# Kernel tuning notes

Measured on AMD Instinct MI355X. Metric: run time of the kernel, lower is better.

The kernel has to match this reference:

```python
import jax, jax.numpy as jnp
import numpy as np

ALPHA = 0.05


def setup_inputs() -> dict:
    key = jax.random.key(0)
    k1, k2, k3, k4 = jax.random.split(key, 4)
    B, C, D = 16384, 4096, 768
    logits = jax.random.normal(k1, (B, C), dtype=jnp.float32)
    targets = jax.random.randint(k2, (B,), 0, C, dtype=jnp.int64)
    prototypes = jax.random.normal(k3, (C, D), dtype=jnp.float32)
    boundaries = jax.random.uniform(k4, (C,), dtype=jnp.float32)
    return {"logits": logits, "targets": targets,
            "prototypes": prototypes, "boundaries": boundaries}


def _cross_entropy(logits, targets):
    # mean over batch of -log_softmax(logits)[target]
    logp = jax.nn.log_softmax(logits, axis=-1)
    nll = -jnp.take_along_axis(logp, targets[:, None], axis=-1)[:, 0]
    return jnp.mean(nll)


def _inter_class_constraint(prototypes, boundaries):
    C = prototypes.shape[0]
    # Gram matrix G[i, j] = p_i . p_j  replaces the O(C^2) python loop
    gram = prototypes @ prototypes.T                      # [C, C]
    diag = jnp.diagonal(gram)                             # p_i . p_i, [C]
    term1 = (1.0 - boundaries) * diag                     # [C], depends on i only
    term2 = (boundaries[None, :] - 1.0) * gram            # [C, C], b_j and G[i,j]
    constraint = term1[:, None] + term2                   # [C, C]
    off_diag = 1.0 - jnp.eye(C, dtype=constraint.dtype)
    ic_sum = jnp.sum(jax.nn.relu(constraint) * off_diag)
    count = C * (C - 1)
    return ic_sum / max(count, 1)


def reference(logits, targets, prototypes, boundaries):
    cls_loss = _cross_entropy(logits, targets)
    ic_loss = _inter_class_constraint(prototypes, boundaries)
    total_loss = cls_loss + ALPHA * ic_loss
    return (total_loss, cls_loss, ic_loss)
```

## Files before the change

kernel.cpp:

```cpp
#include <hip/hip_runtime.h>
#include <hip/hip_bf16.h>

#define NB 16384
#define NC 4096
#define ND 768
#define NT 32
#define NIC 528
#define CE_BLOCKS 2048

#define WS_NLLP 0
#define WS_ICP  16384
#define WS_T1   20480
#define WS_P16  36864


typedef __bf16 bf16x8 __attribute__((ext_vector_type(8)));
typedef float  f32x4  __attribute__((ext_vector_type(4)));

__device__ __forceinline__ unsigned short f2bf(float f) {
    return __builtin_bit_cast(unsigned short, __float2bfloat16(f));
}

template<bool PRECONV>
__global__ __launch_bounds__(256) void prep_kernel(const float* __restrict__ prot,
                                                   const float* __restrict__ bnd,
                                                   float* __restrict__ t1,
                                                   unsigned short* __restrict__ P16) {
    int w = threadIdx.x >> 6;
    int lane = threadIdx.x & 63;
    int row = blockIdx.x * 4 + w;
    const float4* rp = reinterpret_cast<const float4*>(prot + (size_t)row * ND);
    float ss = 0.f;
#pragma unroll
    for (int it = 0; it < 3; ++it) {
        int idx = it * 64 + lane;
        float4 v = rp[idx];
        ss += v.x * v.x + v.y * v.y + v.z * v.z + v.w * v.w;
        if (PRECONV) {
            ushort4 h;
            h.x = f2bf(v.x); h.y = f2bf(v.y); h.z = f2bf(v.z); h.w = f2bf(v.w);
            *reinterpret_cast<ushort4*>(P16 + (size_t)row * ND + idx * 4) = h;
        }
    }
#pragma unroll
    for (int off = 32; off; off >>= 1) ss += __shfl_xor(ss, off);
    if (lane == 0) t1[row] = (1.f - bnd[row]) * ss;
}

__global__ __launch_bounds__(256) void ce_kernel(const float* __restrict__ logits,
                                                 const int* __restrict__ targets,
                                                 double* __restrict__ nllp) {
    const int tid = threadIdx.x;
    const int w = tid >> 6, lane = tid & 63;
    const int b = blockIdx.x;
    float wave_nll = 0.f;
#pragma unroll
    for (int r = 0; r < 2; ++r) {
        const int row = b * 8 + w * 2 + r;
        const int t = targets[row];
        const float4* rp = reinterpret_cast<const float4*>(logits + (size_t)row * NC);
        const float xt = logits[(size_t)row * NC + t];
        float4 v[16];
#pragma unroll
        for (int k = 0; k < 16; ++k) v[k] = rp[lane + 64 * k];
        float m = -3.4e38f;
#pragma unroll
        for (int k = 0; k < 16; ++k)
            m = fmaxf(m, fmaxf(fmaxf(v[k].x, v[k].y), fmaxf(v[k].z, v[k].w)));
#pragma unroll
        for (int off = 32; off; off >>= 1) m = fmaxf(m, __shfl_xor(m, off));
        float s = 0.f;
#pragma unroll
        for (int k = 0; k < 16; ++k)
            s += __expf(v[k].x - m) + __expf(v[k].y - m) + __expf(v[k].z - m) + __expf(v[k].w - m);
#pragma unroll
        for (int off = 32; off; off >>= 1) s += __shfl_xor(s, off);
        wave_nll += m + __logf(s) - xt;
    }
    __shared__ float wp[4];
    if (lane == 0) wp[w] = wave_nll;
    __syncthreads();
    if (tid == 0) nllp[b] = (double)((wp[0] + wp[1]) + (wp[2] + wp[3]));
}

template<bool PRECONV>
__global__ __launch_bounds__(256) void ic_kernel(const unsigned short* __restrict__ P16,
                                                 const float* __restrict__ prot,
                                                 const float* __restrict__ bnd,
                                                 const float* __restrict__ t1,
                                                 float* __restrict__ icp) {
    __shared__ __bf16 As[128][72];
    __shared__ __bf16 Bs[128][72];
    const int tid = threadIdx.x;

    const int icid = blockIdx.x;
    int u = icid, bi = 0;
    while (u >= NT - bi) { u -= NT - bi; ++bi; }
    const int bj = bi + u;
    const bool diag = (bi == bj);
    const int row0 = bi * 128, col0 = bj * 128;

    const int lane = tid & 63, w = tid >> 6;
    const int fr = lane & 15, fq = lane >> 4;
    const int wrow = (w >> 1) * 64, wcol = (w & 1) * 64;

    f32x4 acc[4][4];
#pragma unroll
    for (int mi = 0; mi < 4; ++mi)
#pragma unroll
        for (int nj = 0; nj < 4; ++nj) acc[mi][nj] = (f32x4){0.f, 0.f, 0.f, 0.f};

    for (int kt = 0; kt < ND / 64; ++kt) {
        if (PRECONV) {
#pragma unroll
            for (int s2 = 0; s2 < 4; ++s2) {
                int c = tid + 256 * s2;
                int r = c >> 3, k8 = c & 7;
                uint4 va = *reinterpret_cast<const uint4*>(P16 + (size_t)(row0 + r) * ND + kt * 64 + k8 * 8);
                *reinterpret_cast<uint4*>(&As[r][k8 * 8]) = va;
                uint4 vb = *reinterpret_cast<const uint4*>(P16 + (size_t)(col0 + r) * ND + kt * 64 + k8 * 8);
                *reinterpret_cast<uint4*>(&Bs[r][k8 * 8]) = vb;
            }
        } else {
#pragma unroll
            for (int s2 = 0; s2 < 8; ++s2) {
                int c = tid + 256 * s2;
                int r = c >> 4, k4 = c & 15;
                float4 va = *reinterpret_cast<const float4*>(prot + (size_t)(row0 + r) * ND + kt * 64 + k4 * 4);
                ushort4 ha; ha.x = f2bf(va.x); ha.y = f2bf(va.y); ha.z = f2bf(va.z); ha.w = f2bf(va.w);
                *reinterpret_cast<ushort4*>(&As[r][k4 * 4]) = ha;
                float4 vb = *reinterpret_cast<const float4*>(prot + (size_t)(col0 + r) * ND + kt * 64 + k4 * 4);
                ushort4 hb; hb.x = f2bf(vb.x); hb.y = f2bf(vb.y); hb.z = f2bf(vb.z); hb.w = f2bf(vb.w);
                *reinterpret_cast<ushort4*>(&Bs[r][k4 * 4]) = hb;
            }
        }
        __syncthreads();
#pragma unroll
        for (int ks = 0; ks < 64; ks += 32) {
            bf16x8 af[4], bfv[4];
#pragma unroll
            for (int mi = 0; mi < 4; ++mi)
                af[mi] = *reinterpret_cast<const bf16x8*>(&As[wrow + mi * 16 + fr][ks + fq * 8]);
#pragma unroll
            for (int nj = 0; nj < 4; ++nj)
                bfv[nj] = *reinterpret_cast<const bf16x8*>(&Bs[wcol + nj * 16 + fr][ks + fq * 8]);
#pragma unroll
            for (int mi = 0; mi < 4; ++mi)
#pragma unroll
                for (int nj = 0; nj < 4; ++nj)
                    acc[mi][nj] = __builtin_amdgcn_mfma_f32_16x16x32_bf16(af[mi], bfv[nj], acc[mi][nj], 0, 0, 0);
        }
        __syncthreads();
    }

    float t1a[16], ba1[16];
#pragma unroll
    for (int mi = 0; mi < 4; ++mi)
#pragma unroll
        for (int e = 0; e < 4; ++e) {
            int i = row0 + wrow + mi * 16 + fq * 4 + e;
            t1a[mi * 4 + e] = t1[i];
            ba1[mi * 4 + e] = bnd[i] - 1.f;
        }
    float t1b[4], bb1[4];
#pragma unroll
    for (int nj = 0; nj < 4; ++nj) {
        int j = col0 + wcol + nj * 16 + fr;
        t1b[nj] = t1[j];
        bb1[nj] = bnd[j] - 1.f;
    }

    float sum = 0.f;
#pragma unroll
    for (int mi = 0; mi < 4; ++mi) {
#pragma unroll
        for (int nj = 0; nj < 4; ++nj) {
#pragma unroll
            for (int e = 0; e < 4; ++e) {
                float G = acc[mi][nj][e];
                float tij = t1a[mi * 4 + e] + bb1[nj] * G;
                if (diag) {
                    int il = wrow + mi * 16 + fq * 4 + e;
                    int jl = wcol + nj * 16 + fr;
                    if (il != jl) sum += fmaxf(tij, 0.f);
                } else {
                    float tji = t1b[nj] + ba1[mi * 4 + e] * G;
                    sum += fmaxf(tij, 0.f) + fmaxf(tji, 0.f);
                }
            }
        }
    }
#pragma unroll
    for (int off = 32; off; off >>= 1) sum += __shfl_xor(sum, off);
    __shared__ float redf[4];
    if (lane == 0) redf[w] = sum;
    __syncthreads();
    if (tid == 0) icp[icid] = redf[0] + redf[1] + redf[2] + redf[3];
}

__global__ __launch_bounds__(1024) void fin_kernel(const double* __restrict__ nllp,
                                                   const float* __restrict__ icp,
                                                   float* __restrict__ out) {
    int tid = threadIdx.x;
    double s = nllp[tid] + nllp[tid + 1024];
    double s2 = (tid < NIC) ? (double)icp[tid] : 0.0;
#pragma unroll
    for (int off = 32; off; off >>= 1) {
        s  += __shfl_xor(s, off);
        s2 += __shfl_xor(s2, off);
    }
    __shared__ double sm[16], sm2[16];
    int w = tid >> 6, lane = tid & 63;
    if (lane == 0) { sm[w] = s; sm2[w] = s2; }
    __syncthreads();
    if (tid == 0) {
        double a = 0.0, c = 0.0;
        for (int i = 0; i < 16; ++i) { a += sm[i]; c += sm2[i]; }
        double cls = a / (double)NB;
        double ic  = c / ((double)NC * (double)(NC - 1));
        out[0] = (float)(cls + 0.05 * ic);
        out[1] = (float)cls;
        out[2] = (float)ic;
    }
}

extern "C" void kernel_launch(void* const* d_in, const int* in_sizes, int n_in,
                              void* d_out, int out_size, void* d_ws, size_t ws_size,
                              hipStream_t stream) {
    const float* logits  = (const float*)d_in[0];
    const int*   targets = (const int*)d_in[1];
    const float* prot    = (const float*)d_in[2];
    const float* bnd     = (const float*)d_in[3];
    float* out = (float*)d_out;
    char* ws = (char*)d_ws;
    double* nllp = (double*)(ws + WS_NLLP);
    float* icp = (float*)(ws + WS_ICP);
    float* t1  = (float*)(ws + WS_T1);
    unsigned short* P16 = (unsigned short*)(ws + WS_P16);
    bool pre = ws_size >= (size_t)WS_P16 + 2ull * NC * ND;

    if (pre) {
        prep_kernel<true><<<NC / 4, 256, 0, stream>>>(prot, bnd, t1, P16);
        ic_kernel<true><<<NIC, 256, 0, stream>>>(P16, prot, bnd, t1, icp);
    } else {
        prep_kernel<false><<<NC / 4, 256, 0, stream>>>(prot, bnd, t1, nullptr);
        ic_kernel<false><<<NIC, 256, 0, stream>>>(nullptr, prot, bnd, t1, icp);
    }
    ce_kernel<<<CE_BLOCKS, 256, 0, stream>>>(logits, targets, nllp);
    fin_kernel<<<1, 1024, 0, stream>>>(nllp, icp, out);
}
```

Before: 88.10 us.

## Fuse prototype prep into CE kernel and finalize via atomics in IC kernel

Folds the prototype norm and bf16 conversion work into the cross-entropy kernel, using two of its four waves per block across 2048 blocks. It removes the separate final reduction kernel by having CE and IC blocks atomically accumulate into double accumulators, with a last-block counter writing the outputs. This cuts four launches to a memset plus two kernels. In exchange it adds atomic contention and a memset, and the CE kernel now does extra work before its main loop.

```diff
diff --git a/kernel.cpp b/kernel.cpp
--- a/kernel.cpp
+++ b/kernel.cpp
@@ -8,10 +8,8 @@
 #define NIC 528
 #define CE_BLOCKS 2048
 
-#define WS_NLLP 0
-#define WS_ICP  16384
-#define WS_T1   20480
-#define WS_P16  36864
+#define WS_T1  64
+#define WS_P16 16448
 
 
 typedef __bf16 bf16x8 __attribute__((ext_vector_type(8)));
@@ -22,37 +20,37 @@
 }
 
 template<bool PRECONV>
-__global__ __launch_bounds__(256) void prep_kernel(const float* __restrict__ prot,
-                                                   const float* __restrict__ bnd,
-                                                   float* __restrict__ t1,
-                                                   unsigned short* __restrict__ P16) {
-    int w = threadIdx.x >> 6;
-    int lane = threadIdx.x & 63;
-    int row = blockIdx.x * 4 + w;
-    const float4* rp = reinterpret_cast<const float4*>(prot + (size_t)row * ND);
-    float ss = 0.f;
-#pragma unroll
-    for (int it = 0; it < 3; ++it) {
-        int idx = it * 64 + lane;
-        float4 v = rp[idx];
-        ss += v.x * v.x + v.y * v.y + v.z * v.z + v.w * v.w;
-        if (PRECONV) {
-            ushort4 h;
-            h.x = f2bf(v.x); h.y = f2bf(v.y); h.z = f2bf(v.z); h.w = f2bf(v.w);
-            *reinterpret_cast<ushort4*>(P16 + (size_t)row * ND + idx * 4) = h;
-        }
-    }
-#pragma unroll
-    for (int off = 32; off; off >>= 1) ss += __shfl_xor(ss, off);
-    if (lane == 0) t1[row] = (1.f - bnd[row]) * ss;
-}
-
 __global__ __launch_bounds__(256) void ce_kernel(const float* __restrict__ logits,
                                                  const int* __restrict__ targets,
-                                                 double* __restrict__ nllp) {
+                                                 const float* __restrict__ prot,
+                                                 const float* __restrict__ bnd,
+                                                 float* __restrict__ t1,
+                                                 unsigned short* __restrict__ P16,
+                                                 double* __restrict__ acc_ce) {
     const int tid = threadIdx.x;
     const int w = tid >> 6, lane = tid & 63;
     const int b = blockIdx.x;
+
+    if (w < 2) {
+        const int prow = b * 2 + w;
+        const float4* rp = reinterpret_cast<const float4*>(prot + (size_t)prow * ND);
+        float ss = 0.f;
+#pragma unroll
+        for (int it = 0; it < 3; ++it) {
+            int idx = it * 64 + lane;
+            float4 v = rp[idx];
+            ss += v.x * v.x + v.y * v.y + v.z * v.z + v.w * v.w;
+            if (PRECONV) {
+                ushort4 h;
+                h.x = f2bf(v.x); h.y = f2bf(v.y); h.z = f2bf(v.z); h.w = f2bf(v.w);
+                *reinterpret_cast<ushort4*>(P16 + (size_t)prow * ND + idx * 4) = h;
+            }
+        }
+#pragma unroll
+        for (int off = 32; off; off >>= 1) ss += __shfl_xor(ss, off);
+        if (lane == 0) t1[prow] = (1.f - bnd[prow]) * ss;
+    }
+
     float wave_nll = 0.f;
 #pragma unroll
     for (int r = 0; r < 2; ++r) {
@@ -80,7 +78,8 @@
     __shared__ float wp[4];
     if (lane == 0) wp[w] = wave_nll;
     __syncthreads();
-    if (tid == 0) nllp[b] = (double)((wp[0] + wp[1]) + (wp[2] + wp[3]));
+    if (tid == 0)
+        atomicAdd(acc_ce, (double)((wp[0] + wp[1]) + (wp[2] + wp[3])));
 }
 
 template<bool PRECONV>
@@ -88,7 +87,10 @@
                                                  const float* __restrict__ prot,
                                                  const float* __restrict__ bnd,
                                                  const float* __restrict__ t1,
-                                                 float* __restrict__ icp) {
+                                                 double* __restrict__ acc_ce,
+                                                 double* __restrict__ acc_ic,
+                                                 unsigned int* __restrict__ cnt,
+                                                 float* __restrict__ out) {
     __shared__ __bf16 As[128][72];
     __shared__ __bf16 Bs[128][72];
     const int tid = threadIdx.x;
@@ -195,32 +197,21 @@
     __shared__ float redf[4];
     if (lane == 0) redf[w] = sum;
     __syncthreads();
-    if (tid == 0) icp[icid] = redf[0] + redf[1] + redf[2] + redf[3];
-}
-
-__global__ __launch_bounds__(1024) void fin_kernel(const double* __restrict__ nllp,
-                                                   const float* __restrict__ icp,
-                                                   float* __restrict__ out) {
-    int tid = threadIdx.x;
-    double s = nllp[tid] + nllp[tid + 1024];
-    double s2 = (tid < NIC) ? (double)icp[tid] : 0.0;
-#pragma unroll
-    for (int off = 32; off; off >>= 1) {
-        s  += __shfl_xor(s, off);
-        s2 += __shfl_xor(s2, off);
-    }
-    __shared__ double sm[16], sm2[16];
-    int w = tid >> 6, lane = tid & 63;
-    if (lane == 0) { sm[w] = s; sm2[w] = s2; }
-    __syncthreads();
+
     if (tid == 0) {
-        double a = 0.0, c = 0.0;
-        for (int i = 0; i < 16; ++i) { a += sm[i]; c += sm2[i]; }
-        double cls = a / (double)NB;
-        double ic  = c / ((double)NC * (double)(NC - 1));
-        out[0] = (float)(cls + 0.05 * ic);
-        out[1] = (float)cls;
-        out[2] = (float)ic;
+        atomicAdd(acc_ic, (double)(redf[0] + redf[1] + redf[2] + redf[3]));
+        __threadfence();
+        unsigned int old = atomicAdd(cnt, 1u);
+        if (old == NIC - 1) {
+            __threadfence();
+            double ce_sum = atomicAdd(acc_ce, 0.0);
+            double ic_sum = atomicAdd(acc_ic, 0.0);
+            double cls = ce_sum / (double)NB;
+            double ic  = ic_sum / ((double)NC * (double)(NC - 1));
+            out[0] = (float)(cls + 0.05 * ic);
+            out[1] = (float)cls;
+            out[2] = (float)ic;
+        }
     }
 }
 
@@ -233,19 +224,19 @@
     const float* bnd     = (const float*)d_in[3];
     float* out = (float*)d_out;
     char* ws = (char*)d_ws;
-    double* nllp = (double*)(ws + WS_NLLP);
-    float* icp = (float*)(ws + WS_ICP);
-    float* t1  = (float*)(ws + WS_T1);
+    double* acc_ce = (double*)(ws + 0);
+    double* acc_ic = (double*)(ws + 8);
+    unsigned int* cnt = (unsigned int*)(ws + 16);
+    float* t1 = (float*)(ws + WS_T1);
     unsigned short* P16 = (unsigned short*)(ws + WS_P16);
     bool pre = ws_size >= (size_t)WS_P16 + 2ull * NC * ND;
 
+    hipMemsetAsync(ws, 0, 64, stream);
     if (pre) {
-        prep_kernel<true><<<NC / 4, 256, 0, stream>>>(prot, bnd, t1, P16);
-        ic_kernel<true><<<NIC, 256, 0, stream>>>(P16, prot, bnd, t1, icp);
+        ce_kernel<true><<<CE_BLOCKS, 256, 0, stream>>>(logits, targets, prot, bnd, t1, P16, acc_ce);
+        ic_kernel<true><<<NIC, 256, 0, stream>>>(P16, prot, bnd, t1, acc_ce, acc_ic, cnt, out);
     } else {
-        prep_kernel<false><<<NC / 4, 256, 0, stream>>>(prot, bnd, t1, nullptr);
-        ic_kernel<false><<<NIC, 256, 0, stream>>>(nullptr, prot, bnd, t1, icp);
-    }
-    ce_kernel<<<CE_BLOCKS, 256, 0, stream>>>(logits, targets, nllp);
-    fin_kernel<<<1, 1024, 0, stream>>>(nllp, icp, out);
-}
+        ce_kernel<false><<<CE_BLOCKS, 256, 0, stream>>>(logits, targets, prot, bnd, t1, nullptr, acc_ce);
+        ic_kernel<false><<<NIC, 256, 0, stream>>>(nullptr, prot, bnd, t1, acc_ce, acc_ic, cnt, out);
+    }
+}
```

Result: slower. 108.6 us (+23.3%).

## Use direct global-to-LDS loads with XOR swizzle and fuse final reduction into CE

Applied to the files above, without the earlier changes.

The IC GEMM tile loads now use global_load_lds 16-byte transfers straight into LDS, and the LDS tiles are unpadded with an XOR swizzle to avoid bank conflicts. The separate finalize kernel is removed: the CE kernel's last block, found through an atomic counter reset in the prep kernel, does the final reduction. The aim is fewer register round-trips for tile staging and one fewer kernel launch. In exchange it relies on threadfence and atomic ordering, and each CE block now does an extra atomic.

```diff
diff --git a/kernel.cpp b/kernel.cpp
--- a/kernel.cpp
+++ b/kernel.cpp
@@ -6,12 +6,13 @@
 #define ND 768
 #define NT 32
 #define NIC 528
-#define CE_BLOCKS 2048
-
-#define WS_NLLP 0
-#define WS_ICP  16384
-#define WS_T1   20480
-#define WS_P16  36864
+#define CEB 2048
+
+#define WS_CNT  0
+#define WS_NLLP 64
+#define WS_ICP  16448
+#define WS_T1   18560
+#define WS_P16  34944
 
 
 typedef __bf16 bf16x8 __attribute__((ext_vector_type(8)));
@@ -19,13 +20,21 @@
 
 __device__ __forceinline__ unsigned short f2bf(float f) {
     return __builtin_bit_cast(unsigned short, __float2bfloat16(f));
+}
+
+__device__ __forceinline__ void gload16(const void* g, void* l) {
+    __builtin_amdgcn_global_load_lds(
+        (const __attribute__((address_space(1))) unsigned int*)g,
+        (__attribute__((address_space(3))) unsigned int*)l, 16, 0, 0);
 }
 
 template<bool PRECONV>
 __global__ __launch_bounds__(256) void prep_kernel(const float* __restrict__ prot,
                                                    const float* __restrict__ bnd,
                                                    float* __restrict__ t1,
-                                                   unsigned short* __restrict__ P16) {
+                                                   unsigned short* __restrict__ P16,
+                                                   unsigned int* __restrict__ cnt) {
+    if (blockIdx.x == 0 && threadIdx.x == 0) *cnt = 0u;
     int w = threadIdx.x >> 6;
     int lane = threadIdx.x & 63;
     int row = blockIdx.x * 4 + w;
@@ -47,50 +56,15 @@
     if (lane == 0) t1[row] = (1.f - bnd[row]) * ss;
 }
 
-__global__ __launch_bounds__(256) void ce_kernel(const float* __restrict__ logits,
-                                                 const int* __restrict__ targets,
-                                                 double* __restrict__ nllp) {
-    const int tid = threadIdx.x;
-    const int w = tid >> 6, lane = tid & 63;
-    const int b = blockIdx.x;
-    float wave_nll = 0.f;
-#pragma unroll
-    for (int r = 0; r < 2; ++r) {
-        const int row = b * 8 + w * 2 + r;
-        const int t = targets[row];
-        const float4* rp = reinterpret_cast<const float4*>(logits + (size_t)row * NC);
-        const float xt = logits[(size_t)row * NC + t];
-        float4 v[16];
-#pragma unroll
-        for (int k = 0; k < 16; ++k) v[k] = rp[lane + 64 * k];
-        float m = -3.4e38f;
-#pragma unroll
-        for (int k = 0; k < 16; ++k)
-            m = fmaxf(m, fmaxf(fmaxf(v[k].x, v[k].y), fmaxf(v[k].z, v[k].w)));
-#pragma unroll
-        for (int off = 32; off; off >>= 1) m = fmaxf(m, __shfl_xor(m, off));
-        float s = 0.f;
-#pragma unroll
-        for (int k = 0; k < 16; ++k)
-            s += __expf(v[k].x - m) + __expf(v[k].y - m) + __expf(v[k].z - m) + __expf(v[k].w - m);
-#pragma unroll
-        for (int off = 32; off; off >>= 1) s += __shfl_xor(s, off);
-        wave_nll += m + __logf(s) - xt;
-    }
-    __shared__ float wp[4];
-    if (lane == 0) wp[w] = wave_nll;
-    __syncthreads();
-    if (tid == 0) nllp[b] = (double)((wp[0] + wp[1]) + (wp[2] + wp[3]));
-}
-
 template<bool PRECONV>
 __global__ __launch_bounds__(256) void ic_kernel(const unsigned short* __restrict__ P16,
                                                  const float* __restrict__ prot,
                                                  const float* __restrict__ bnd,
                                                  const float* __restrict__ t1,
                                                  float* __restrict__ icp) {
-    __shared__ __bf16 As[128][72];
-    __shared__ __bf16 Bs[128][72];
+    __shared__ __bf16 As[128][64];
+    __shared__ __bf16 Bs[128][64];
+    __shared__ float redf[4];
     const int tid = threadIdx.x;
 
     const int icid = blockIdx.x;
@@ -104,6 +78,9 @@
     const int fr = lane & 15, fq = lane >> 4;
     const int wrow = (w >> 1) * 64, wcol = (w & 1) * 64;
 
+    char* ldsA = (char*)&As[0][0];
+    char* ldsB = (char*)&Bs[0][0];
+
     f32x4 acc[4][4];
 #pragma unroll
     for (int mi = 0; mi < 4; ++mi)
@@ -113,37 +90,53 @@
     for (int kt = 0; kt < ND / 64; ++kt) {
         if (PRECONV) {
 #pragma unroll
+            for (int it = 0; it < 4; ++it) {
+                int base = (w * 4 + it) * 1024;
+                int r = (base >> 7) + (lane >> 3);
+                int cbl = lane & 7;
+                int cbs = cbl ^ (r & 7);
+                const unsigned short* ga = P16 + (size_t)(row0 + r) * ND + kt * 64 + cbs * 8;
+                gload16(ga, ldsA + base);
+                const unsigned short* gb = P16 + (size_t)(col0 + r) * ND + kt * 64 + cbs * 8;
+                gload16(gb, ldsB + base);
+            }
+        } else {
+#pragma unroll
             for (int s2 = 0; s2 < 4; ++s2) {
                 int c = tid + 256 * s2;
-                int r = c >> 3, k8 = c & 7;
-                uint4 va = *reinterpret_cast<const uint4*>(P16 + (size_t)(row0 + r) * ND + kt * 64 + k8 * 8);
-                *reinterpret_cast<uint4*>(&As[r][k8 * 8]) = va;
-                uint4 vb = *reinterpret_cast<const uint4*>(P16 + (size_t)(col0 + r) * ND + kt * 64 + k8 * 8);
-                *reinterpret_cast<uint4*>(&Bs[r][k8 * 8]) = vb;
-            }
-        } else {
-#pragma unroll
-            for (int s2 = 0; s2 < 8; ++s2) {
-                int c = tid + 256 * s2;
-                int r = c >> 4, k4 = c & 15;
-                float4 va = *reinterpret_cast<const float4*>(prot + (size_t)(row0 + r) * ND + kt * 64 + k4 * 4);
-                ushort4 ha; ha.x = f2bf(va.x); ha.y = f2bf(va.y); ha.z = f2bf(va.z); ha.w = f2bf(va.w);
-                *reinterpret_cast<ushort4*>(&As[r][k4 * 4]) = ha;
-                float4 vb = *reinterpret_cast<const float4*>(prot + (size_t)(col0 + r) * ND + kt * 64 + k4 * 4);
-                ushort4 hb; hb.x = f2bf(vb.x); hb.y = f2bf(vb.y); hb.z = f2bf(vb.z); hb.w = f2bf(vb.w);
-                *reinterpret_cast<ushort4*>(&Bs[r][k4 * 4]) = hb;
+                int r = c >> 3, cb = c & 7;
+                int swz = (cb ^ (r & 7)) << 4;
+                const float4* pa = reinterpret_cast<const float4*>(prot + (size_t)(row0 + r) * ND + kt * 64 + cb * 8);
+                float4 a0 = pa[0], a1 = pa[1];
+                ushort4 h0, h1;
+                h0.x = f2bf(a0.x); h0.y = f2bf(a0.y); h0.z = f2bf(a0.z); h0.w = f2bf(a0.w);
+                h1.x = f2bf(a1.x); h1.y = f2bf(a1.y); h1.z = f2bf(a1.z); h1.w = f2bf(a1.w);
+                *reinterpret_cast<ushort4*>(ldsA + r * 128 + swz) = h0;
+                *reinterpret_cast<ushort4*>(ldsA + r * 128 + swz + 8) = h1;
+                const float4* pb = reinterpret_cast<const float4*>(prot + (size_t)(col0 + r) * ND + kt * 64 + cb * 8);
+                float4 b0 = pb[0], b1 = pb[1];
+                ushort4 g0, g1;
+                g0.x = f2bf(b0.x); g0.y = f2bf(b0.y); g0.z = f2bf(b0.z); g0.w = f2bf(b0.w);
+                g1.x = f2bf(b1.x); g1.y = f2bf(b1.y); g1.z = f2bf(b1.z); g1.w = f2bf(b1.w);
+                *reinterpret_cast<ushort4*>(ldsB + r * 128 + swz) = g0;
+                *reinterpret_cast<ushort4*>(ldsB + r * 128 + swz + 8) = g1;
             }
         }
         __syncthreads();
 #pragma unroll
         for (int ks = 0; ks < 64; ks += 32) {
+            const int cb0 = fq + (ks >> 3);
             bf16x8 af[4], bfv[4];
 #pragma unroll
-            for (int mi = 0; mi < 4; ++mi)
-                af[mi] = *reinterpret_cast<const bf16x8*>(&As[wrow + mi * 16 + fr][ks + fq * 8]);
-#pragma unroll
-            for (int nj = 0; nj < 4; ++nj)
-                bfv[nj] = *reinterpret_cast<const bf16x8*>(&Bs[wcol + nj * 16 + fr][ks + fq * 8]);
+            for (int mi = 0; mi < 4; ++mi) {
+                int r = wrow + mi * 16 + fr;
+                af[mi] = *reinterpret_cast<const bf16x8*>(ldsA + r * 128 + ((cb0 ^ (r & 7)) << 4));
+            }
+#pragma unroll
+            for (int nj = 0; nj < 4; ++nj) {
+                int r = wcol + nj * 16 + fr;
+                bfv[nj] = *reinterpret_cast<const bf16x8*>(ldsB + r * 128 + ((cb0 ^ (r & 7)) << 4));
+            }
 #pragma unroll
             for (int mi = 0; mi < 4; ++mi)
 #pragma unroll
@@ -192,30 +185,74 @@
     }
 #pragma unroll
     for (int off = 32; off; off >>= 1) sum += __shfl_xor(sum, off);
-    __shared__ float redf[4];
     if (lane == 0) redf[w] = sum;
     __syncthreads();
     if (tid == 0) icp[icid] = redf[0] + redf[1] + redf[2] + redf[3];
 }
 
-__global__ __launch_bounds__(1024) void fin_kernel(const double* __restrict__ nllp,
-                                                   const float* __restrict__ icp,
-                                                   float* __restrict__ out) {
-    int tid = threadIdx.x;
-    double s = nllp[tid] + nllp[tid + 1024];
-    double s2 = (tid < NIC) ? (double)icp[tid] : 0.0;
+__global__ __launch_bounds__(256) void ce_kernel(const float* __restrict__ logits,
+                                                 const int* __restrict__ targets,
+                                                 double* __restrict__ nllp,
+                                                 const float* __restrict__ icp,
+                                                 unsigned int* __restrict__ cnt,
+                                                 float* __restrict__ out) {
+    const int tid = threadIdx.x;
+    const int w = tid >> 6, lane = tid & 63;
+    const int b = blockIdx.x;
+    float wave_nll = 0.f;
+#pragma unroll
+    for (int r = 0; r < 2; ++r) {
+        const int row = b * 8 + w * 2 + r;
+        const int t = targets[row];
+        const float4* rp = reinterpret_cast<const float4*>(logits + (size_t)row * NC);
+        const float xt = logits[(size_t)row * NC + t];
+        float4 v[16];
+#pragma unroll
+        for (int k = 0; k < 16; ++k) v[k] = rp[lane + 64 * k];
+        float m = -3.4e38f;
+#pragma unroll
+        for (int k = 0; k < 16; ++k)
+            m = fmaxf(m, fmaxf(fmaxf(v[k].x, v[k].y), fmaxf(v[k].z, v[k].w)));
+#pragma unroll
+        for (int off = 32; off; off >>= 1) m = fmaxf(m, __shfl_xor(m, off));
+        float s = 0.f;
+#pragma unroll
+        for (int k = 0; k < 16; ++k)
+            s += __expf(v[k].x - m) + __expf(v[k].y - m) + __expf(v[k].z - m) + __expf(v[k].w - m);
+#pragma unroll
+        for (int off = 32; off; off >>= 1) s += __shfl_xor(s, off);
+        wave_nll += m + __logf(s) - xt;
+    }
+    __shared__ float wp[4];
+    __shared__ int sWin;
+    if (lane == 0) wp[w] = wave_nll;
+    __syncthreads();
+    if (tid == 0) {
+        nllp[b] = (double)((wp[0] + wp[1]) + (wp[2] + wp[3]));
+        __threadfence();
+        unsigned int old = atomicAdd(cnt, 1u);
+        sWin = (old == CEB - 1);
+    }
+    __syncthreads();
+    if (!sWin) return;
+
+    __threadfence();
+    double s = 0.0;
+#pragma unroll
+    for (int k = 0; k < 8; ++k) s += nllp[tid + 256 * k];
+    double s2 = (double)icp[tid] + (double)icp[tid + 256];
+    if (tid < 16) s2 += (double)icp[512 + tid];
 #pragma unroll
     for (int off = 32; off; off >>= 1) {
         s  += __shfl_xor(s, off);
         s2 += __shfl_xor(s2, off);
     }
-    __shared__ double sm[16], sm2[16];
-    int w = tid >> 6, lane = tid & 63;
+    __shared__ double sm[4], sm2[4];
     if (lane == 0) { sm[w] = s; sm2[w] = s2; }
     __syncthreads();
     if (tid == 0) {
-        double a = 0.0, c = 0.0;
-        for (int i = 0; i < 16; ++i) { a += sm[i]; c += sm2[i]; }
+        double a = sm[0] + sm[1] + sm[2] + sm[3];
+        double c = sm2[0] + sm2[1] + sm2[2] + sm2[3];
         double cls = a / (double)NB;
         double ic  = c / ((double)NC * (double)(NC - 1));
         out[0] = (float)(cls + 0.05 * ic);
@@ -233,6 +270,7 @@
     const float* bnd     = (const float*)d_in[3];
     float* out = (float*)d_out;
     char* ws = (char*)d_ws;
+    unsigned int* cnt = (unsigned int*)(ws + WS_CNT);
     double* nllp = (double*)(ws + WS_NLLP);
     float* icp = (float*)(ws + WS_ICP);
     float* t1  = (float*)(ws + WS_T1);
@@ -240,12 +278,11 @@
     bool pre = ws_size >= (size_t)WS_P16 + 2ull * NC * ND;
 
     if (pre) {
-        prep_kernel<true><<<NC / 4, 256, 0, stream>>>(prot, bnd, t1, P16);
+        prep_kernel<true><<<NC / 4, 256, 0, stream>>>(prot, bnd, t1, P16, cnt);
         ic_kernel<true><<<NIC, 256, 0, stream>>>(P16, prot, bnd, t1, icp);
     } else {
-        prep_kernel<false><<<NC / 4, 256, 0, stream>>>(prot, bnd, t1, nullptr);
+        prep_kernel<false><<<NC / 4, 256, 0, stream>>>(prot, bnd, t1, nullptr, cnt);
         ic_kernel<false><<<NIC, 256, 0, stream>>>(nullptr, prot, bnd, t1, icp);
     }
-    ce_kernel<<<CE_BLOCKS, 256, 0, stream>>>(logits, targets, nllp);
-    fin_kernel<<<1, 1024, 0, stream>>>(nllp, icp, out);
-}
+    ce_kernel<<<CEB, 256, 0, stream>>>(logits, targets, nllp, icp, cnt, out);
+}
```

After: 172.5 us. +95.8%, slower.

## Double-buffer IC GEMM tiles with direct global-to-LDS loads and XOR swizzle

Applied to the files above, without the earlier changes.

The prototype Gram-matrix kernel now uses two LDS buffers and loads bf16 tiles straight into shared memory with global_load_lds, prefetching the next K-slice while MFMAs run on the current one. The padded LDS layout is replaced with an XOR swizzle on 16-byte chunks to avoid bank conflicts without padding. This aims to hide global memory latency and drop the register round-trip and one barrier per K step. It doubles LDS use, which may lower occupancy, and depends on the asynchronous LDS load finishing before the barrier.

```diff
diff --git a/kernel.cpp b/kernel.cpp
--- a/kernel.cpp
+++ b/kernel.cpp
@@ -6,12 +6,12 @@
 #define ND 768
 #define NT 32
 #define NIC 528
-#define CE_BLOCKS 2048
+#define CEB 2048
 
 #define WS_NLLP 0
 #define WS_ICP  16384
-#define WS_T1   20480
-#define WS_P16  36864
+#define WS_T1   18560
+#define WS_P16  34944
 
 
 typedef __bf16 bf16x8 __attribute__((ext_vector_type(8)));
@@ -19,6 +19,12 @@
 
 __device__ __forceinline__ unsigned short f2bf(float f) {
     return __builtin_bit_cast(unsigned short, __float2bfloat16(f));
+}
+
+__device__ __forceinline__ void gload16(const void* g, void* l) {
+    __builtin_amdgcn_global_load_lds(
+        (const __attribute__((address_space(1))) unsigned int*)g,
+        (__attribute__((address_space(3))) unsigned int*)l, 16, 0, 0);
 }
 
 template<bool PRECONV>
@@ -47,50 +53,15 @@
     if (lane == 0) t1[row] = (1.f - bnd[row]) * ss;
 }
 
-__global__ __launch_bounds__(256) void ce_kernel(const float* __restrict__ logits,
-                                                 const int* __restrict__ targets,
-                                                 double* __restrict__ nllp) {
-    const int tid = threadIdx.x;
-    const int w = tid >> 6, lane = tid & 63;
-    const int b = blockIdx.x;
-    float wave_nll = 0.f;
-#pragma unroll
-    for (int r = 0; r < 2; ++r) {
-        const int row = b * 8 + w * 2 + r;
-        const int t = targets[row];
-        const float4* rp = reinterpret_cast<const float4*>(logits + (size_t)row * NC);
-        const float xt = logits[(size_t)row * NC + t];
-        float4 v[16];
-#pragma unroll
-        for (int k = 0; k < 16; ++k) v[k] = rp[lane + 64 * k];
-        float m = -3.4e38f;
-#pragma unroll
-        for (int k = 0; k < 16; ++k)
-            m = fmaxf(m, fmaxf(fmaxf(v[k].x, v[k].y), fmaxf(v[k].z, v[k].w)));
-#pragma unroll
-        for (int off = 32; off; off >>= 1) m = fmaxf(m, __shfl_xor(m, off));
-        float s = 0.f;
-#pragma unroll
-        for (int k = 0; k < 16; ++k)
-            s += __expf(v[k].x - m) + __expf(v[k].y - m) + __expf(v[k].z - m) + __expf(v[k].w - m);
-#pragma unroll
-        for (int off = 32; off; off >>= 1) s += __shfl_xor(s, off);
-        wave_nll += m + __logf(s) - xt;
-    }
-    __shared__ float wp[4];
-    if (lane == 0) wp[w] = wave_nll;
-    __syncthreads();
-    if (tid == 0) nllp[b] = (double)((wp[0] + wp[1]) + (wp[2] + wp[3]));
-}
-
 template<bool PRECONV>
 __global__ __launch_bounds__(256) void ic_kernel(const unsigned short* __restrict__ P16,
                                                  const float* __restrict__ prot,
                                                  const float* __restrict__ bnd,
                                                  const float* __restrict__ t1,
                                                  float* __restrict__ icp) {
-    __shared__ __bf16 As[128][72];
-    __shared__ __bf16 Bs[128][72];
+    __shared__ __bf16 As[2][128][64];
+    __shared__ __bf16 Bs[2][128][64];
+    __shared__ float redf[4];
     const int tid = threadIdx.x;
 
     const int icid = blockIdx.x;
@@ -104,53 +75,110 @@
     const int fr = lane & 15, fq = lane >> 4;
     const int wrow = (w >> 1) * 64, wcol = (w & 1) * 64;
 
+    char* ldsA = (char*)&As[0][0][0];
+    char* ldsB = (char*)&Bs[0][0][0];
+    const int BUFB = 128 * 64 * 2;
+
     f32x4 acc[4][4];
 #pragma unroll
     for (int mi = 0; mi < 4; ++mi)
 #pragma unroll
         for (int nj = 0; nj < 4; ++nj) acc[mi][nj] = (f32x4){0.f, 0.f, 0.f, 0.f};
 
-    for (int kt = 0; kt < ND / 64; ++kt) {
-        if (PRECONV) {
+    if (PRECONV) {
+        const int rloc = lane >> 3;
+        const int cbl = lane & 7;
+#pragma unroll
+        for (int it = 0; it < 4; ++it) {
+            int base = (w * 4 + it) * 1024;
+            int r = (base >> 7) + rloc;
+            int cbs = cbl ^ (r & 7);
+            gload16(P16 + (size_t)(row0 + r) * ND + cbs * 8, ldsA + base);
+            gload16(P16 + (size_t)(col0 + r) * ND + cbs * 8, ldsB + base);
+        }
+        __syncthreads();
+#pragma unroll
+        for (int kt = 0; kt < 6; ++kt) {
+            const int cur = (kt & 1) * BUFB;
+            if (kt < 5) {
+                const int nxt = ((kt + 1) & 1) * BUFB;
+#pragma unroll
+                for (int it = 0; it < 4; ++it) {
+                    int base = (w * 4 + it) * 1024;
+                    int r = (base >> 7) + rloc;
+                    int cbs = cbl ^ (r & 7);
+                    gload16(P16 + (size_t)(row0 + r) * ND + (kt + 1) * 64 + cbs * 8, ldsA + nxt + base);
+                    gload16(P16 + (size_t)(col0 + r) * ND + (kt + 1) * 64 + cbs * 8, ldsB + nxt + base);
+                }
+            }
+#pragma unroll
+            for (int ks = 0; ks < 64; ks += 32) {
+                const int cb0 = fq + (ks >> 3);
+                bf16x8 af[4], bfv[4];
+#pragma unroll
+                for (int mi = 0; mi < 4; ++mi) {
+                    int r = wrow + mi * 16 + fr;
+                    af[mi] = *reinterpret_cast<const bf16x8*>(ldsA + cur + r * 128 + ((cb0 ^ (r & 7)) << 4));
+                }
+#pragma unroll
+                for (int nj = 0; nj < 4; ++nj) {
+                    int r = wcol + nj * 16 + fr;
+                    bfv[nj] = *reinterpret_cast<const bf16x8*>(ldsB + cur + r * 128 + ((cb0 ^ (r & 7)) << 4));
+                }
+#pragma unroll
+                for (int mi = 0; mi < 4; ++mi)
+#pragma unroll
+                    for (int nj = 0; nj < 4; ++nj)
+                        acc[mi][nj] = __builtin_amdgcn_mfma_f32_16x16x32_bf16(af[mi], bfv[nj], acc[mi][nj], 0, 0, 0);
+            }
+            __syncthreads();
+        }
+    } else {
+        for (int kt = 0; kt < 6; ++kt) {
+            const int cur = (kt & 1) * BUFB;
 #pragma unroll
             for (int s2 = 0; s2 < 4; ++s2) {
                 int c = tid + 256 * s2;
-                int r = c >> 3, k8 = c & 7;
-                uint4 va = *reinterpret_cast<const uint4*>(P16 + (size_t)(row0 + r) * ND + kt * 64 + k8 * 8);
-                *reinterpret_cast<uint4*>(&As[r][k8 * 8]) = va;
-                uint4 vb = *reinterpret_cast<const uint4*>(P16 + (size_t)(col0 + r) * ND + kt * 64 + k8 * 8);
-                *reinterpret_cast<uint4*>(&Bs[r][k8 * 8]) = vb;
-            }
-        } else {
-#pragma unroll
-            for (int s2 = 0; s2 < 8; ++s2) {
-                int c = tid + 256 * s2;
-                int r = c >> 4, k4 = c & 15;
-                float4 va = *reinterpret_cast<const float4*>(prot + (size_t)(row0 + r) * ND + kt * 64 + k4 * 4);
-                ushort4 ha; ha.x = f2bf(va.x); ha.y = f2bf(va.y); ha.z = f2bf(va.z); ha.w = f2bf(va.w);
-                *reinterpret_cast<ushort4*>(&As[r][k4 * 4]) = ha;
-                float4 vb = *reinterpret_cast<const float4*>(prot + (size_t)(col0 + r) * ND + kt * 64 + k4 * 4);
-                ushort4 hb; hb.x = f2bf(vb.x); hb.y = f2bf(vb.y); hb.z = f2bf(vb.z); hb.w = f2bf(vb.w);
-                *reinterpret_cast<ushort4*>(&Bs[r][k4 * 4]) = hb;
-            }
-        }
-        __syncthreads();
-#pragma unroll
-        for (int ks = 0; ks < 64; ks += 32) {
-            bf16x8 af[4], bfv[4];
-#pragma unroll
-            for (int mi = 0; mi < 4; ++mi)
-                af[mi] = *reinterpret_cast<const bf16x8*>(&As[wrow + mi * 16 + fr][ks + fq * 8]);
-#pragma unroll
-            for (int nj = 0; nj < 4; ++nj)
-                bfv[nj] = *reinterpret_cast<const bf16x8*>(&Bs[wcol + nj * 16 + fr][ks + fq * 8]);
-#pragma unroll
-            for (int mi = 0; mi < 4; ++mi)
-#pragma unroll
-                for (int nj = 0; nj < 4; ++nj)
-                    acc[mi][nj] = __builtin_amdgcn_mfma_f32_16x16x32_bf16(af[mi], bfv[nj], acc[mi][nj], 0, 0, 0);
-        }
-        __syncthreads();
+                int r = c >> 3, cb = c & 7;
+                int swz = ((cb ^ (r & 7)) << 4);
+                const float4* pa = reinterpret_cast<const float4*>(prot + (size_t)(row0 + r) * ND + kt * 64 + cb * 8);
+                float4 a0 = pa[0], a1 = pa[1];
+                ushort4 h0, h1;
+                h0.x = f2bf(a0.x); h0.y = f2bf(a0.y); h0.z = f2bf(a0.z); h0.w = f2bf(a0.w);
+                h1.x = f2bf(a1.x); h1.y = f2bf(a1.y); h1.z = f2bf(a1.z); h1.w = f2bf(a1.w);
+                *reinterpret_cast<ushort4*>(ldsA + cur + r * 128 + swz) = h0;
+                *reinterpret_cast<ushort4*>(ldsA + cur + r * 128 + swz + 8) = h1;
+                const float4* pb = reinterpret_cast<const float4*>(prot + (size_t)(col0 + r) * ND + kt * 64 + cb * 8);
+                float4 b0 = pb[0], b1 = pb[1];
+                ushort4 g0, g1;
+                g0.x = f2bf(b0.x); g0.y = f2bf(b0.y); g0.z = f2bf(b0.z); g0.w = f2bf(b0.w);
+                g1.x = f2bf(b1.x); g1.y = f2bf(b1.y); g1.z = f2bf(b1.z); g1.w = f2bf(b1.w);
+                *reinterpret_cast<ushort4*>(ldsB + cur + r * 128 + swz) = g0;
+                *reinterpret_cast<ushort4*>(ldsB + cur + r * 128 + swz + 8) = g1;
+            }
+            __syncthreads();
+#pragma unroll
+            for (int ks = 0; ks < 64; ks += 32) {
+                const int cb0 = fq + (ks >> 3);
+                bf16x8 af[4], bfv[4];
+#pragma unroll
+                for (int mi = 0; mi < 4; ++mi) {
+                    int r = wrow + mi * 16 + fr;
+                    af[mi] = *reinterpret_cast<const bf16x8*>(ldsA + cur + r * 128 + ((cb0 ^ (r & 7)) << 4));
+                }
+#pragma unroll
+                for (int nj = 0; nj < 4; ++nj) {
+                    int r = wcol + nj * 16 + fr;
+                    bfv[nj] = *reinterpret_cast<const bf16x8*>(ldsB + cur + r * 128 + ((cb0 ^ (r & 7)) << 4));
+                }
+#pragma unroll
+                for (int mi = 0; mi < 4; ++mi)
+#pragma unroll
+                    for (int nj = 0; nj < 4; ++nj)
+                        acc[mi][nj] = __builtin_amdgcn_mfma_f32_16x16x32_bf16(af[mi], bfv[nj], acc[mi][nj], 0, 0, 0);
+            }
+            __syncthreads();
+        }
     }
 
     float t1a[16], ba1[16];
@@ -192,10 +220,45 @@
     }
 #pragma unroll
     for (int off = 32; off; off >>= 1) sum += __shfl_xor(sum, off);
-    __shared__ float redf[4];
     if (lane == 0) redf[w] = sum;
     __syncthreads();
     if (tid == 0) icp[icid] = redf[0] + redf[1] + redf[2] + redf[3];
+}
+
+__global__ __launch_bounds__(256) void ce_kernel(const float* __restrict__ logits,
+                                                 const int* __restrict__ targets,
+                                                 double* __restrict__ nllp) {
+    const int tid = threadIdx.x;
+    const int w = tid >> 6, lane = tid & 63;
+    const int b = blockIdx.x;
+    float wave_nll = 0.f;
+#pragma unroll
+    for (int r = 0; r < 2; ++r) {
+        const int row = b * 8 + w * 2 + r;
+        const int t = targets[row];
+        const float4* rp = reinterpret_cast<const float4*>(logits + (size_t)row * NC);
+        const float xt = logits[(size_t)row * NC + t];
+        float4 v[16];
+#pragma unroll
+        for (int k = 0; k < 16; ++k) v[k] = rp[lane + 64 * k];
+        float m = -3.4e38f;
+#pragma unroll
+        for (int k = 0; k < 16; ++k)
+            m = fmaxf(m, fmaxf(fmaxf(v[k].x, v[k].y), fmaxf(v[k].z, v[k].w)));
+#pragma unroll
+        for (int off = 32; off; off >>= 1) m = fmaxf(m, __shfl_xor(m, off));
+        float s = 0.f;
+#pragma unroll
+        for (int k = 0; k < 16; ++k)
+            s += __expf(v[k].x - m) + __expf(v[k].y - m) + __expf(v[k].z - m) + __expf(v[k].w - m);
+#pragma unroll
+        for (int off = 32; off; off >>= 1) s += __shfl_xor(s, off);
+        wave_nll += m + __logf(s) - xt;
+    }
+    __shared__ float wp[4];
+    if (lane == 0) wp[w] = wave_nll;
+    __syncthreads();
+    if (tid == 0) nllp[b] = (double)((wp[0] + wp[1]) + (wp[2] + wp[3]));
 }
 
 __global__ __launch_bounds__(1024) void fin_kernel(const double* __restrict__ nllp,
@@ -246,6 +309,6 @@
         prep_kernel<false><<<NC / 4, 256, 0, stream>>>(prot, bnd, t1, nullptr);
         ic_kernel<false><<<NIC, 256, 0, stream>>>(nullptr, prot, bnd, t1, icp);
     }
-    ce_kernel<<<CE_BLOCKS, 256, 0, stream>>>(logits, targets, nllp);
+    ce_kernel<<<CEB, 256, 0, stream>>>(logits, targets, nllp);
     fin_kernel<<<1, 1024, 0, stream>>>(nllp, icp, out);
 }
```

Result: faster. 71.53 us, median of 2 (-18.8%).
